# Kernel tuning notes

Measured on AMD Instinct MI355X. Metric: run time of the kernel, lower is better.

The kernel has to match this reference:

```python
import jax, jax.numpy as jnp
import numpy as np

# FeedForwardQuantum: per-token circuit is RX(x_i) then RY(theta_i) on wire i,
# measure PauliZ on each wire. Starting from |0...0> the state stays a product
# state and single-qubit algebra gives <Z_i> = cos(x_i) * cos(theta_i).
# Head: linear(n_qubits->ffn) -> relu -> linear(ffn->embed). Dropout is eval-mode identity.


def setup_inputs() -> dict:
    key = jax.random.key(0)
    ks = jax.random.split(key, 6)
    B, S, E, F, Q = 8, 4096, 512, 2048, 8
    return {
        "x": jax.random.normal(ks[0], (B, S, E), dtype=jnp.float32),
        "theta": jax.random.normal(ks[1], (Q,), dtype=jnp.float32),
        "W1": jax.random.normal(ks[2], (F, Q), dtype=jnp.float32) * 0.1,
        "b1": jax.random.normal(ks[3], (F,), dtype=jnp.float32) * 0.1,
        "W2": jax.random.normal(ks[4], (E, F), dtype=jnp.float32) * 0.02,
        "b2": jax.random.normal(ks[5], (E,), dtype=jnp.float32) * 0.02,
    }


def reference(x, theta, W1, b1, W2, b2):
    Q = theta.shape[0]
    # Quantum layer: <Z_i> = cos(x_i) * cos(theta_i)   [B, S, Q]
    q = jnp.cos(x[..., :Q]) * jnp.cos(theta)
    h = jax.nn.relu(jnp.einsum('bsq,fq->bsf', q, W1) + b1)  # [B, S, F]
    return jnp.einsum('bsf,ef->bse', h, W2) + b2            # [B, S, E]
```

## Files before the change

### kernel.cpp

```cpp
#include <hip/hip_runtime.h>

typedef unsigned short u16;
typedef short bf16x8 __attribute__((ext_vector_type(8)));
typedef u16 u16x8 __attribute__((ext_vector_type(8)));
typedef float f32x4 __attribute__((ext_vector_type(4)));

__device__ __forceinline__ u16 f2bf_rne(float f) {
  unsigned u = __builtin_bit_cast(unsigned, f);
  unsigned r = (u + 0x7fffu + ((u >> 16) & 1u)) >> 16;
  return (u16)r;
}

#define GLDS16(g, l) __builtin_amdgcn_global_load_lds(                        \
    (const __attribute__((address_space(1))) unsigned int*)(g),               \
    (__attribute__((address_space(3))) unsigned int*)(l), 16, 0, 0)

#define NKP 32

__global__ void k_w2prep(const float* __restrict__ W2, u16* __restrict__ dst) {
  int i = blockIdx.x * blockDim.x + threadIdx.x;
  int jj  = i & 7;
  int ph  = (i >> 3) & 7;
  int col = (i >> 6) & 127;
  int kp  = (i >> 13) & 31;
  int nt  = (i >> 18) & 3;
  int f = (kp << 6) + ((ph ^ (col & 7)) << 3) + jj;
  int e = (nt << 7) + col;
  dst[i] = f2bf_rne(W2[(e << 11) + f]);
}

__global__ __launch_bounds__(256, 3) void k_ffq(
    const float* __restrict__ x, const float* __restrict__ theta,
    const u16* __restrict__ w2arr,
    const float* __restrict__ W1, const float* __restrict__ b1,
    const float* __restrict__ b2, float* __restrict__ out)
{
  __shared__ __align__(16) char smem[49152];
  char* sA  = smem;
  char* sB0 = smem + 16384;
  char* sB1 = smem + 32768;

  const int tid  = threadIdx.x;
  const int lane = tid & 63;
  const int wid  = tid >> 6;
  const int nt = blockIdx.x & 3;
  const int mt = blockIdx.x >> 2;

  const int myt = ((wid & 1) << 6) | lane;
  const int fo0 = __builtin_amdgcn_readfirstlane((wid >> 1) << 2);
  float qr[8];
  {
    const float4* xp = (const float4*)(x + (size_t)((mt << 7) + myt) * 512);
    const float4 x0 = xp[0], x1 = xp[1];
    const float4* tp = (const float4*)theta;
    const float4 t0 = tp[0], t1 = tp[1];
    qr[0] = cosf(x0.x) * cosf(t0.x);  qr[1] = cosf(x0.y) * cosf(t0.y);
    qr[2] = cosf(x0.z) * cosf(t0.z);  qr[3] = cosf(x0.w) * cosf(t0.w);
    qr[4] = cosf(x1.x) * cosf(t1.x);  qr[5] = cosf(x1.y) * cosf(t1.y);
    qr[6] = cosf(x1.z) * cosf(t1.z);  qr[7] = cosf(x1.w) * cosf(t1.w);
  }
  int wA[4];
#pragma unroll
  for (int g = 0; g < 4; ++g)
    wA[g] = (myt << 7) + (((fo0 + g) ^ (myt & 7)) << 4);

  const int wr = wid >> 1, wc = wid & 1;
  const int l15 = lane & 15;
  const int kq  = lane >> 4;

  f32x4 acc[4][4];
#pragma unroll
  for (int i = 0; i < 4; ++i)
#pragma unroll
    for (int j = 0; j < 4; ++j) acc[i][j] = (f32x4){0.f, 0.f, 0.f, 0.f};

  u16x8 hN[4];
  auto computeH = [&](int kt) {
#pragma unroll
    for (int g = 0; g < 4; ++g) {
      const int f0 = (kt << 6) + ((fo0 + g) << 3);
      const float* __restrict__ bp = b1 + f0;
#pragma unroll
      for (int r = 0; r < 8; ++r) {
        const float* __restrict__ wp = W1 + ((f0 + r) << 3);
        float s = bp[r];
        s = fmaf(qr[0], wp[0], s); s = fmaf(qr[1], wp[1], s);
        s = fmaf(qr[2], wp[2], s); s = fmaf(qr[3], wp[3], s);
        s = fmaf(qr[4], wp[4], s); s = fmaf(qr[5], wp[5], s);
        s = fmaf(qr[6], wp[6], s); s = fmaf(qr[7], wp[7], s);
        hN[g][r] = f2bf_rne(fmaxf(s, 0.f));
      }
    }
  };

  auto writeA = [&]() {
#pragma unroll
    for (int g = 0; g < 4; ++g)
      *(u16x8*)(sA + wA[g]) = hN[g];
  };

  auto stageB = [&](int kt, char* dst) {
    const char* src = (const char*)w2arr + ((size_t)((nt << 5) + kt) << 14);
#pragma unroll
    for (int i = 0; i < 4; ++i) {
      const int off = ((i << 2) | wid) << 10;
      GLDS16(src + off + lane * 16, dst + off);
    }
  };

  stageB(0, sB0);
  computeH(0);
  writeA();
  __syncthreads();

  for (int kp = 0; kp < NKP; ++kp) {
    char* sBc = (kp & 1) ? sB1 : sB0;
    char* sBn = (kp & 1) ? sB0 : sB1;
    const bool pre = (kp < NKP - 1);
    if (pre) stageB(kp + 1, sBn);
    __builtin_amdgcn_s_setprio(1);
#pragma unroll
    for (int ks = 0; ks < 2; ++ks) {
      const int o = (ks << 2) | kq;
      bf16x8 ah[4];
#pragma unroll
      for (int mi = 0; mi < 4; ++mi) {
        const int arow = (wr << 6) | (mi << 4) | l15;
        ah[mi] = *(const bf16x8*)(sA + (arow << 7) + ((o ^ (arow & 7)) << 4));
      }
#pragma unroll
      for (int ni = 0; ni < 4; ++ni) {
        const int bcol = (wc << 6) | (ni << 4) | l15;
        const bf16x8 bh = *(const bf16x8*)(sBc + (bcol << 7) + ((o ^ (bcol & 7)) << 4));
#pragma unroll
        for (int mi = 0; mi < 4; ++mi)
          acc[mi][ni] = __builtin_amdgcn_mfma_f32_16x16x32_bf16(ah[mi], bh, acc[mi][ni], 0, 0, 0);
      }
    }
    __builtin_amdgcn_s_setprio(0);
    if (pre) {
      computeH(kp + 1);
      __syncthreads();
      writeA();
      __syncthreads();
    }
  }

#pragma unroll
  for (int ni = 0; ni < 4; ++ni) {
    const int col = (nt << 7) | (wc << 6) | (ni << 4) | l15;
    const float bv = b2[col];
#pragma unroll
    for (int mi = 0; mi < 4; ++mi) {
      const int row0 = (mt << 7) | (wr << 6) | (mi << 4) | (kq << 2);
      float* op = out + (size_t)row0 * 512 + col;
#pragma unroll
      for (int r = 0; r < 4; ++r)
        op[(size_t)r * 512] = acc[mi][ni][r] + bv;
    }
  }
}

extern "C" void kernel_launch(void* const* d_in, const int* in_sizes, int n_in,
                              void* d_out, int out_size, void* d_ws, size_t ws_size,
                              hipStream_t stream) {
  const float* x     = (const float*)d_in[0];
  const float* theta = (const float*)d_in[1];
  const float* W1    = (const float*)d_in[2];
  const float* b1    = (const float*)d_in[3];
  const float* W2    = (const float*)d_in[4];
  const float* b2    = (const float*)d_in[5];
  float* out = (float*)d_out;

  const int M = in_sizes[0] / 512;
  u16* w2arr = (u16*)d_ws;

  k_w2prep<<<(1 << 20) / 256, 256, 0, stream>>>(W2, w2arr);
  k_ffq<<<dim3((M / 128) * 4), 256, 0, stream>>>(x, theta, w2arr, W1, b1, b2, out);
}
```

Measured before the change: 288.3 us.

## Split hidden activation computation into separate kernel and stream H via LDS

The fused kernel recomputed the small first layer (relu(q·W1+b1)) inside the GEMM loop, redundantly across the four N tiles and serialized with extra barriers. Now a separate kernel materializes H in bf16 in workspace, in a swizzled layout, and the GEMM kernel double-buffers both A and B tiles with global-to-LDS loads. The GEMM also remaps blocks across XCD-like groups of 8, and the M dimension is chunked to fit the workspace. This removes 4x redundant H compute and per-step synchronization, at the cost of 64MB of extra HBM write/read traffic and lower occupancy from 64KB of LDS.

```diff
diff --git a/kernel.cpp b/kernel.cpp
--- a/kernel.cpp
+++ b/kernel.cpp
@@ -15,8 +15,6 @@
     (const __attribute__((address_space(1))) unsigned int*)(g),               \
     (__attribute__((address_space(3))) unsigned int*)(l), 16, 0, 0)
 
-#define NKP 32
-
 __global__ void k_w2prep(const float* __restrict__ W2, u16* __restrict__ dst) {
   int i = blockIdx.x * blockDim.x + threadIdx.x;
   int jj  = i & 7;
@@ -29,28 +27,19 @@
   dst[i] = f2bf_rne(W2[(e << 11) + f]);
 }
 
-__global__ __launch_bounds__(256, 3) void k_ffq(
+__global__ __launch_bounds__(256) void k_h(
     const float* __restrict__ x, const float* __restrict__ theta,
-    const u16* __restrict__ w2arr,
     const float* __restrict__ W1, const float* __restrict__ b1,
-    const float* __restrict__ b2, float* __restrict__ out)
+    u16* __restrict__ Hws, int mbase, int chunkM)
 {
-  __shared__ __align__(16) char smem[49152];
-  char* sA  = smem;
-  char* sB0 = smem + 16384;
-  char* sB1 = smem + 32768;
+  const int lane = threadIdx.x & 63;
+  const int w    = threadIdx.x >> 6;
+  const int tok  = (blockIdx.x << 6) + lane;
+  const int obase = __builtin_amdgcn_readfirstlane(w << 6);
 
-  const int tid  = threadIdx.x;
-  const int lane = tid & 63;
-  const int wid  = tid >> 6;
-  const int nt = blockIdx.x & 3;
-  const int mt = blockIdx.x >> 2;
-
-  const int myt = ((wid & 1) << 6) | lane;
-  const int fo0 = __builtin_amdgcn_readfirstlane((wid >> 1) << 2);
   float qr[8];
   {
-    const float4* xp = (const float4*)(x + (size_t)((mt << 7) + myt) * 512);
+    const float4* xp = (const float4*)(x + (size_t)(mbase + tok) * 512);
     const float4 x0 = xp[0], x1 = xp[1];
     const float4* tp = (const float4*)theta;
     const float4 t0 = tp[0], t1 = tp[1];
@@ -59,14 +48,53 @@
     qr[4] = cosf(x1.x) * cosf(t1.x);  qr[5] = cosf(x1.y) * cosf(t1.y);
     qr[6] = cosf(x1.z) * cosf(t1.z);  qr[7] = cosf(x1.w) * cosf(t1.w);
   }
-  int wA[4];
+
+#pragma unroll 2
+  for (int i = 0; i < 64; ++i) {
+    const int oct = obase + i;
+    const int f0 = oct << 3;
+    const float* __restrict__ bp = b1 + f0;
+    u16x8 h8;
 #pragma unroll
-  for (int g = 0; g < 4; ++g)
-    wA[g] = (myt << 7) + (((fo0 + g) ^ (myt & 7)) << 4);
+    for (int r = 0; r < 8; ++r) {
+      const float* __restrict__ wp = W1 + ((f0 + r) << 3);
+      float s = bp[r];
+      s = fmaf(qr[0], wp[0], s); s = fmaf(qr[1], wp[1], s);
+      s = fmaf(qr[2], wp[2], s); s = fmaf(qr[3], wp[3], s);
+      s = fmaf(qr[4], wp[4], s); s = fmaf(qr[5], wp[5], s);
+      s = fmaf(qr[6], wp[6], s); s = fmaf(qr[7], wp[7], s);
+      h8[r] = f2bf_rne(fmaxf(s, 0.f));
+    }
+    *(u16x8*)(Hws + (((size_t)oct * chunkM + tok) << 3)) = h8;
+  }
+}
+
+__global__ __launch_bounds__(256, 2) void k_gemm(
+    const u16* __restrict__ Hws, const u16* __restrict__ w2arr,
+    const float* __restrict__ b2, float* __restrict__ out,
+    int mbase, int chunkM, int qper)
+{
+  __shared__ __align__(16) char smem[65536];
+  char* sA0 = smem;
+  char* sA1 = smem + 16384;
+  char* sB0 = smem + 32768;
+  char* sB1 = smem + 49152;
+
+  const int lane = threadIdx.x & 63;
+  const int wid  = threadIdx.x >> 6;
+
+  const int vb = (blockIdx.x & 7) * qper + (blockIdx.x >> 3);
+  const int mt = vb >> 2;
+  const int nt = vb & 3;
 
   const int wr = wid >> 1, wc = wid & 1;
   const int l15 = lane & 15;
   const int kq  = lane >> 4;
+
+  const int op = (lane & 7) ^ ((lane >> 3) & 7);
+  const char* asrc0 = (const char*)Hws +
+      ((((size_t)op * chunkM + ((size_t)mt << 7) + (lane >> 3)) << 4));
+  const size_t akp = ((size_t)chunkM << 7);
 
   f32x4 acc[4][4];
 #pragma unroll
@@ -74,31 +102,14 @@
 #pragma unroll
     for (int j = 0; j < 4; ++j) acc[i][j] = (f32x4){0.f, 0.f, 0.f, 0.f};
 
-  u16x8 hN[4];
-  auto computeH = [&](int kt) {
+  auto stageA = [&](int kt, char* dst) {
+    const char* src = asrc0 + (size_t)kt * akp;
 #pragma unroll
-    for (int g = 0; g < 4; ++g) {
-      const int f0 = (kt << 6) + ((fo0 + g) << 3);
-      const float* __restrict__ bp = b1 + f0;
-#pragma unroll
-      for (int r = 0; r < 8; ++r) {
-        const float* __restrict__ wp = W1 + ((f0 + r) << 3);
-        float s = bp[r];
-        s = fmaf(qr[0], wp[0], s); s = fmaf(qr[1], wp[1], s);
-        s = fmaf(qr[2], wp[2], s); s = fmaf(qr[3], wp[3], s);
-        s = fmaf(qr[4], wp[4], s); s = fmaf(qr[5], wp[5], s);
-        s = fmaf(qr[6], wp[6], s); s = fmaf(qr[7], wp[7], s);
-        hN[g][r] = f2bf_rne(fmaxf(s, 0.f));
-      }
+    for (int i = 0; i < 4; ++i) {
+      const int c = (i << 2) | wid;
+      GLDS16(src + c * 128, dst + (c << 10));
     }
   };
-
-  auto writeA = [&]() {
-#pragma unroll
-    for (int g = 0; g < 4; ++g)
-      *(u16x8*)(sA + wA[g]) = hN[g];
-  };
-
   auto stageB = [&](int kt, char* dst) {
     const char* src = (const char*)w2arr + ((size_t)((nt << 5) + kt) << 14);
 #pragma unroll
@@ -108,16 +119,19 @@
     }
   };
 
+  stageA(0, sA0);
   stageB(0, sB0);
-  computeH(0);
-  writeA();
   __syncthreads();
 
-  for (int kp = 0; kp < NKP; ++kp) {
+  for (int kp = 0; kp < 32; ++kp) {
+    char* sAc = (kp & 1) ? sA1 : sA0;
+    char* sAn = (kp & 1) ? sA0 : sA1;
     char* sBc = (kp & 1) ? sB1 : sB0;
     char* sBn = (kp & 1) ? sB0 : sB1;
-    const bool pre = (kp < NKP - 1);
-    if (pre) stageB(kp + 1, sBn);
+    if (kp < 31) {
+      stageA(kp + 1, sAn);
+      stageB(kp + 1, sBn);
+    }
     __builtin_amdgcn_s_setprio(1);
 #pragma unroll
     for (int ks = 0; ks < 2; ++ks) {
@@ -126,7 +140,7 @@
 #pragma unroll
       for (int mi = 0; mi < 4; ++mi) {
         const int arow = (wr << 6) | (mi << 4) | l15;
-        ah[mi] = *(const bf16x8*)(sA + (arow << 7) + ((o ^ (arow & 7)) << 4));
+        ah[mi] = *(const bf16x8*)(sAc + (arow << 7) + ((o ^ (arow & 7)) << 4));
       }
 #pragma unroll
       for (int ni = 0; ni < 4; ++ni) {
@@ -138,12 +152,7 @@
       }
     }
     __builtin_amdgcn_s_setprio(0);
-    if (pre) {
-      computeH(kp + 1);
-      __syncthreads();
-      writeA();
-      __syncthreads();
-    }
+    __syncthreads();
   }
 
 #pragma unroll
@@ -152,11 +161,11 @@
     const float bv = b2[col];
 #pragma unroll
     for (int mi = 0; mi < 4; ++mi) {
-      const int row0 = (mt << 7) | (wr << 6) | (mi << 4) | (kq << 2);
-      float* op = out + (size_t)row0 * 512 + col;
+      const int row0 = mbase + (mt << 7) + ((wr << 6) | (mi << 4) | (kq << 2));
+      float* op2 = out + (size_t)row0 * 512 + col;
 #pragma unroll
       for (int r = 0; r < 4; ++r)
-        op[(size_t)r * 512] = acc[mi][ni][r] + bv;
+        op2[(size_t)r * 512] = acc[mi][ni][r] + bv;
     }
   }
 }
@@ -173,8 +182,18 @@
   float* out = (float*)d_out;
 
   const int M = in_sizes[0] / 512;
+
   u16* w2arr = (u16*)d_ws;
+  u16* Hws   = (u16*)((char*)d_ws + (2u << 20));
+  size_t avail = (ws_size > (2u << 20)) ? ws_size - (2u << 20) : 0;
+
+  int chunkM = M;
+  while (chunkM > 1024 && (size_t)chunkM * 4096 > avail) chunkM >>= 1;
 
   k_w2prep<<<(1 << 20) / 256, 256, 0, stream>>>(W2, w2arr);
-  k_ffq<<<dim3((M / 128) * 4), 256, 0, stream>>>(x, theta, w2arr, W1, b1, b2, out);
+  for (int mb = 0; mb < M; mb += chunkM) {
+    k_h<<<chunkM / 64, 256, 0, stream>>>(x, theta, W1, b1, Hws, mb, chunkM);
+    const int nb = (chunkM / 128) * 4;
+    k_gemm<<<nb, 256, 0, stream>>>(Hws, w2arr, b2, out, mb, chunkM, nb / 8);
+  }
 }
```

Result: faster. 250.6 us (-13.1%).
